# Kernel optimization log

Measured on AMD Instinct MI355X. Metric: run time of the kernel, lower is better.

Reference implementation:

```python
import jax, jax.numpy as jnp
import numpy as np

V, A, L = 10000, 600, 6          # dx vocab, num ancestors, ancestors-per-leaf
O, E = 128, 128                  # ontoEmbDim, EHREmbDim
ATD, PTD, DPL = 128, 128, 500    # ontoattnDim, ptattnDim, dpLabelSize
B, T, N = 64, 32, 40             # batch, visits, codes-per-visit


def _l2norm(x):
    return x / jnp.maximum(jnp.linalg.norm(x, axis=-1, keepdims=True), 1e-12)


def setup_inputs() -> dict:
    key = jax.random.key(0)
    ks = jax.random.split(key, 16)
    g = lambda k, shape, fan: (jax.random.normal(k, shape) / np.sqrt(fan)).astype(jnp.float32)
    dxseqs = jax.random.randint(ks[0], (B, T, N), 0, V + 1)          # V = padding idx
    dx_onehot = jax.random.uniform(ks[1], (T, B, V), dtype=jnp.float32)
    leaves = jax.random.randint(ks[2], (V, L), 0, V)
    ancestors = jax.random.randint(ks[3], (V, L), V, V + A)
    ehr_table = g(ks[4], (V + 1, E), E).at[V].set(0.0)               # padding row zero
    return dict(
        dxseqs=dxseqs, dx_onehot=dx_onehot, leaves=leaves, ancestors=ancestors,
        onto_table=g(ks[5], (V + A, O), O),
        onto_Wa=g(ks[6], (2 * O, ATD), 2 * O), onto_ba=jnp.zeros((ATD,), jnp.float32),
        onto_Wc=g(ks[7], (ATD, 1), ATD), onto_bc=jnp.zeros((1,), jnp.float32),
        ehr_table=ehr_table,
        attn_W=g(ks[8], (2 * E + 2 * O, PTD), 2 * E + 2 * O), attn_b=jnp.zeros((PTD,), jnp.float32),
        comb_W=g(ks[9], (PTD, 1), PTD), comb_b=jnp.zeros((1,), jnp.float32),
        co_W=g(ks[10], (E, V), E), co_b=jnp.zeros((V,), jnp.float32),
        dp_W=g(ks[11], (O + E, DPL), O + E), dp_b=jnp.zeros((DPL,), jnp.float32),
    )


def _forward(dxseqs, dx_onehot, leaves, ancestors, onto_table, onto_Wa, onto_ba,
             onto_Wc, onto_bc, ehr_table, attn_W, attn_b, comb_W, comb_b,
             co_W, co_b, dp_W, dp_b):
    # --- OntoEmb (GRAM-style ancestor attention) ---
    el = onto_table[leaves]                                  # (V, L, O)
    ea = onto_table[ancestors]                               # (V, L, O)
    h = jnp.tanh(jnp.concatenate([el, ea], -1) @ onto_Wa + onto_ba)
    a = jax.nn.softmax(h @ onto_Wc + onto_bc, axis=1)        # (V, L, 1)
    onto_all = jnp.concatenate(
        [jnp.sum(a * ea, axis=1), jnp.zeros((1, O), onto_table.dtype)], axis=0)  # (V+1, O)

    dxOnto = onto_all[dxseqs]                                # (B, T, N, O)
    ontoV = jnp.einsum('tbv,vo->bto', dx_onehot, onto_all[:-1])  # (B, T, O)
    dxEHR = ehr_table[dxseqs]                                # (B, T, N, E)
    ehrV = _l2norm(jnp.sum(dxEHR, axis=2))                   # (B, T, E)

    # --- cooccurrence branch ---
    cooccurU = jax.nn.softmax(ehrV @ co_W + co_b, axis=2)    # (B, T, V)
    vonehot = jnp.transpose(dx_onehot, (1, 0, 2))            # (B, T, V)
    cooccur_loss = -jnp.mean(jnp.sum(vonehot * jnp.log(cooccurU), axis=(1, 2)))

    # --- additive (Bahdanau) attention over codes in a visit ---
    dxEmb = jnp.concatenate([dxEHR, dxOnto], -1)             # (B, T, N, E+O)
    vs = jnp.concatenate([ontoV, ehrV], -1)[:, :, None, :]   # (B, T, 1, O+E)
    attnInput = jnp.concatenate([jnp.broadcast_to(vs, dxEmb.shape), dxEmb], -1)
    mlp = jnp.tanh(attnInput @ attn_W + attn_b)              # (B, T, N, PTD)
    attn = jax.nn.softmax(mlp @ comb_W + comb_b, axis=2)     # (B, T, N, 1)
    vs2 = jnp.sum(attn * dxEmb, axis=2)                      # (B, T, E+O)

    dp = jax.nn.softmax(jnp.tanh(_l2norm(vs2)) @ dp_W + dp_b, axis=2)  # (B, T, DPL)
    return dp, cooccur_loss * 10.0


def reference(dxseqs, dx_onehot, leaves, ancestors, onto_table, onto_Wa, onto_ba,
              onto_Wc, onto_bc, ehr_table, attn_W, attn_b, comb_W, comb_b,
              co_W, co_b, dp_W, dp_b):
    return _forward(dxseqs, dx_onehot, leaves, ancestors, onto_table, onto_Wa, onto_ba,
                    onto_Wc, onto_bc, ehr_table, attn_W, attn_b, comb_W, comb_b,
                    co_W, co_b, dp_W, dp_b)
```

## Files before the change

kernel.cpp:

```cpp
#include <hip/hip_runtime.h>
#include <math.h>

typedef float4 f4;
typedef __bf16 bf16x8 __attribute__((ext_vector_type(8)));
typedef float f32x4 __attribute__((ext_vector_type(4)));

static constexpr int kV = 10000, kL = 6, kDPL = 500;
static constexpr int kB = 64, kT = 32, kN = 40, kBT = 2048;
static constexpr int kXC = 5;
static constexpr int kNB = 272;
static constexpr int kLd = 10240;
static constexpr int kNP = 313;
static constexpr int kVT2 = 40;

#define MFMA16 __builtin_amdgcn_mfma_f32_16x16x32_bf16

typedef const __attribute__((address_space(1))) unsigned int ga_u32;
typedef __attribute__((address_space(3))) unsigned int lds_u32;
__device__ __forceinline__ void gll16(const float* g, float* l) {
  __builtin_amdgcn_global_load_lds((ga_u32*)g, (lds_u32*)l, 16, 0, 0);
}

__device__ __forceinline__ bf16x8 cvt8(f4 a, f4 b) {
  bf16x8 r;
  r[0] = (__bf16)a.x; r[1] = (__bf16)a.y; r[2] = (__bf16)a.z; r[3] = (__bf16)a.w;
  r[4] = (__bf16)b.x; r[5] = (__bf16)b.y; r[6] = (__bf16)b.z; r[7] = (__bf16)b.w;
  return r;
}

__global__ __launch_bounds__(256) void mmore_cvt_bf16(
    const float* __restrict__ in, __bf16* __restrict__ out, int n) {
  int i = (blockIdx.x * 256 + threadIdx.x) * 8;
  if (i < n) {
    f4 a = *(const f4*)(in + i), b = *(const f4*)(in + i + 4);
    *(bf16x8*)(out + i) = cvt8(a, b);
  }
}

__global__ __launch_bounds__(256) void mmore_trcvt(
    const float* __restrict__ in, __bf16* __restrict__ out,
    int K, int N, int Kpad) {
  int t = threadIdx.x;
  int n = blockIdx.y * 16 + (t & 15);
  int kb = (blockIdx.x * 16 + (t >> 4)) * 8;
  bf16x8 r;
  #pragma unroll
  for (int i = 0; i < 8; ++i) {
    int k = kb + i;
    float v = (k < K && n < N) ? in[(size_t)k * N + n] : 0.f;
    r[i] = (__bf16)v;
  }
  *(bf16x8*)(out + (size_t)n * Kpad + kb) = r;
}

__global__ __launch_bounds__(256) void mmore_brow(
    const float* __restrict__ coW, const float* __restrict__ cob,
    __bf16* __restrict__ Btab) {
  int id = blockIdx.x * 256 + threadIdx.x;
  int rr = id / 1280;
  int kk = (id - rr * 1280) * 8;
  bf16x8 r;
  #pragma unroll
  for (int i = 0; i < 8; ++i) {
    int k = kk + i;
    float v = 0.f;
    if (k < kV) {
      if (rr < 128) v = coW[(size_t)rr * kV + k];
      else if (rr == 128) v = cob[k];
      else if (rr == 129) v = 1.f;
    }
    r[i] = (__bf16)v;
  }
  *(bf16x8*)(Btab + (size_t)(128 + rr) * kLd + kk) = r;
}

__global__ __launch_bounds__(256) void mmore_panelize(
    const __bf16* __restrict__ Btab, __bf16* __restrict__ Bp) {
  int t = threadIdx.x;
  int S = blockIdx.x, ry = blockIdx.y;
  int row = ry * 16 + (t >> 4), kk = (t & 15) * 2;
  unsigned v = *(const unsigned*)(Btab + (size_t)row * kLd + S * 32 + kk);
  *(unsigned*)(Bp + ((size_t)S * kNB + row) * 32 + kk) = v;
}

__global__ __launch_bounds__(128) void mmore_ehrv(
    const int* __restrict__ dxseqs, const float* __restrict__ ehr_table,
    float* __restrict__ ehrV) {
  int bt = blockIdx.x, t = threadIdx.x;
  const int* row = dxseqs + bt * kN;
  float acc = 0.f;
  for (int n = 0; n < kN; ++n) acc += ehr_table[(size_t)row[n] * 128 + t];
  float v = acc * acc;
  #pragma unroll
  for (int off = 32; off; off >>= 1) v += __shfl_down(v, off);
  __shared__ float red[2];
  if ((t & 63) == 0) red[t >> 6] = v;
  __syncthreads();
  float ss = red[0] + red[1];
  float inv = 1.f / fmaxf(sqrtf(ss), 1e-12f);
  ehrV[bt * 128 + t] = acc * inv;
}

__global__ __launch_bounds__(256) void mmore_scores_mfma(
    const __bf16* __restrict__ otb, const int* __restrict__ leaves,
    const int* __restrict__ anc, const __bf16* __restrict__ WaT,
    const float* __restrict__ ba, const float* __restrict__ Wc,
    const float* __restrict__ bc, float* __restrict__ s_out) {
  int t = threadIdx.x, wave = t >> 6, lane = t & 63, lm = lane & 15, lg = lane >> 4;
  int r0 = blockIdx.x * 32;
  int rA0 = r0 + lm, rA1 = rA0 + 16;
  int v0 = rA0 / 6, l0 = rA0 - v0 * 6, v1 = rA1 / 6, l1 = rA1 - v1 * 6;
  const __bf16* pL0 = otb + (size_t)leaves[v0 * 6 + l0] * 128;
  const __bf16* pA0 = otb + (size_t)anc[v0 * 6 + l0] * 128;
  const __bf16* pL1 = otb + (size_t)leaves[v1 * 6 + l1] * 128;
  const __bf16* pA1 = otb + (size_t)anc[v1 * 6 + l1] * 128;
  const __bf16* bp = WaT + (size_t)(wave * 32 + lm) * 256 + lg * 8;
  f32x4 acc[2][2] = {};
  #pragma unroll
  for (int kb = 0; kb < 256; kb += 32) {
    int k = kb + lg * 8;
    const __bf16* s0 = (k < 128) ? (pL0 + k) : (pA0 + (k - 128));
    const __bf16* s1 = (k < 128) ? (pL1 + k) : (pA1 + (k - 128));
    bf16x8 a0 = *(const bf16x8*)s0;
    bf16x8 a1 = *(const bf16x8*)s1;
    bf16x8 b0 = *(const bf16x8*)(bp + kb);
    bf16x8 b1 = *(const bf16x8*)(bp + kb + 16 * 256);
    acc[0][0] = MFMA16(a0, b0, acc[0][0], 0, 0, 0);
    acc[0][1] = MFMA16(a0, b1, acc[0][1], 0, 0, 0);
    acc[1][0] = MFMA16(a1, b0, acc[1][0], 0, 0, 0);
    acc[1][1] = MFMA16(a1, b1, acc[1][1], 0, 0, 0);
  }
  __shared__ float red[4][32];
  float bcv = bc[0];
  #pragma unroll
  for (int mf = 0; mf < 2; ++mf) {
    #pragma unroll
    for (int j = 0; j < 4; ++j) {
      float p = 0.f;
      #pragma unroll
      for (int nf = 0; nf < 2; ++nf) {
        int c = wave * 32 + nf * 16 + lm;
        p += tanhf(acc[mf][nf][j] + ba[c]) * Wc[c];
      }
      #pragma unroll
      for (int off = 8; off; off >>= 1) p += __shfl_xor(p, off);
      if (lm == 0) red[wave][mf * 16 + lg * 4 + j] = p;
    }
  }
  __syncthreads();
  if (t < 32) s_out[r0 + t] = red[0][t] + red[1][t] + red[2][t] + red[3][t] + bcv;
}

__global__ __launch_bounds__(128) void mmore_onto(
    const float* __restrict__ ot, const int* __restrict__ anc,
    const float* __restrict__ s_in, float* __restrict__ onto_all) {
  int v = blockIdx.x, t = threadIdx.x;
  if (v == kV) { onto_all[(size_t)v * 128 + t] = 0.f; return; }
  __shared__ float sv[kL];
  __shared__ int aidx[kL];
  if (t < kL) { sv[t] = s_in[v * kL + t]; aidx[t] = anc[v * kL + t]; }
  __syncthreads();
  float mx = sv[0];
  #pragma unroll
  for (int l = 1; l < kL; ++l) mx = fmaxf(mx, sv[l]);
  float e[kL], sum = 0.f;
  #pragma unroll
  for (int l = 0; l < kL; ++l) { e[l] = expf(sv[l] - mx); sum += e[l]; }
  float acc = 0.f;
  #pragma unroll
  for (int l = 0; l < kL; ++l)
    acc += (e[l] / sum) * ot[(size_t)aidx[l] * 128 + t];
  onto_all[(size_t)v * 128 + t] = acc;
}

__global__ __launch_bounds__(256) void mmore_xgemm(
    const float* __restrict__ X, const __bf16* __restrict__ Bp,
    float* __restrict__ part) {
  __shared__ __align__(16) float Xs[2][16][256];
  int t = threadIdx.x, w = t >> 6, lane = t & 63, lm = lane & 15, lg = lane >> 4;
  int bid = blockIdx.x;
  int swz = (bid & 7) * 80 + (bid >> 3);
  int btile = swz & 127, chunk = swz >> 7;
  int r0 = btile * 16;
  bool lastc = (chunk == kXC - 1);
  int nSS = lastc ? 7 : 8;
  int kbase = chunk * 2048;
  int f0 = w * 4;
  const __bf16* bp = Bp + ((size_t)(chunk * 64) * kNB + lm) * 32 + lg * 8;
  f32x4 acc[5] = {};

#define XGV6_STAGE(db, S)                                                     \
  {                                                                           \
    _Pragma("unroll")                                                         \
    for (int u = 0; u < 4; ++u) {                                             \
      int row_ = w * 4 + u;                                                   \
      const float* src_ = X + (size_t)(r0 + row_) * kV + kbase + (S) * 256 +  \
                          ((lane ^ (row_ & 7)) << 2);                         \
      gll16(src_, &Xs[db][row_][0]);                                          \
    }                                                                         \
  }

  XGV6_STAGE(0, 0);
  asm volatile("s_waitcnt vmcnt(0)" ::: "memory");
  __builtin_amdgcn_s_barrier();
  int buf = 0;
  for (int S = 0; S < nSS; ++S) {
    if (S + 1 < nSS) {
      if (buf == 0) { XGV6_STAGE(1, S + 1); } else { XGV6_STAGE(0, S + 1); }
    }
    #pragma unroll
    for (int j = 0; j < 8; ++j) {
      int G0 = 8 * j + 2 * lg;
      int sw0 = G0 ^ (lm & 7), sw1 = (G0 + 1) ^ (lm & 7);
      f4 x0 = *(const f4*)&Xs[buf][lm][sw0 * 4];
      f4 x1 = *(const f4*)&Xs[buf][lm][sw1 * 4];
      bf16x8 af = cvt8(x0, x1);
      const __bf16* bs = bp + (size_t)(S * 8 + j) * (kNB * 32);
      acc[0] = MFMA16(af, *(const bf16x8*)(bs + (f0 + 0) * 512), acc[0], 0, 0, 0);
      acc[1] = MFMA16(af, *(const bf16x8*)(bs + (f0 + 1) * 512), acc[1], 0, 0, 0);
      acc[2] = MFMA16(af, *(const bf16x8*)(bs + (f0 + 2) * 512), acc[2], 0, 0, 0);
      acc[3] = MFMA16(af, *(const bf16x8*)(bs + (f0 + 3) * 512), acc[3], 0, 0, 0);
      if (w == 3)
        acc[4] = MFMA16(af, *(const bf16x8*)(bs + 16 * 512), acc[4], 0, 0, 0);
    }
    asm volatile("s_waitcnt vmcnt(0)" ::: "memory");
    __builtin_amdgcn_s_barrier();
    buf ^= 1;
  }
  if (lastc) {
    f4 z = make_float4(0.f, 0.f, 0.f, 0.f), x0 = z, x1 = z;
    if (lg < 2) {
      const float* xp = X + (size_t)(r0 + lm) * kV + 9984 + lg * 8;
      x0 = *(const f4*)xp; x1 = *(const f4*)(xp + 4);
    }
    bf16x8 af = cvt8(x0, x1);
    const __bf16* bs = Bp + ((size_t)312 * kNB + lm) * 32 + lg * 8;
    acc[0] = MFMA16(af, *(const bf16x8*)(bs + (f0 + 0) * 512), acc[0], 0, 0, 0);
    acc[1] = MFMA16(af, *(const bf16x8*)(bs + (f0 + 1) * 512), acc[1], 0, 0, 0);
    acc[2] = MFMA16(af, *(const bf16x8*)(bs + (f0 + 2) * 512), acc[2], 0, 0, 0);
    acc[3] = MFMA16(af, *(const bf16x8*)(bs + (f0 + 3) * 512), acc[3], 0, 0, 0);
    if (w == 3)
      acc[4] = MFMA16(af, *(const bf16x8*)(bs + 16 * 512), acc[4], 0, 0, 0);
  }
  #pragma unroll
  for (int j = 0; j < 4; ++j) {
    int r = r0 + lg * 4 + j;
    int bt = (r & 63) * kT + (r >> 6);
    size_t o = ((size_t)chunk * kBT + bt) * kNB;
    #pragma unroll
    for (int f = 0; f < 4; ++f) part[o + (f0 + f) * 16 + lm] = acc[f][j];
    if (w == 3) part[o + 256 + lm] = acc[4][j];
  }
#undef XGV6_STAGE
}

__global__ __launch_bounds__(256) void mmore_creduce(
    const float* __restrict__ part, float* __restrict__ ontoV,
    float* __restrict__ pwred, float* __restrict__ pc, float* __restrict__ sp) {
  int bt = blockIdx.x, t = threadIdx.x;
  for (int c = t; c < kNB; c += 256) {
    float a = 0.f;
    #pragma unroll
    for (int ch = 0; ch < kXC; ++ch)
      a += part[((size_t)ch * kBT + bt) * kNB + c];
    if (c < 128) ontoV[(size_t)bt * 128 + c] = a;
    else if (c < 256) pwred[(size_t)bt * 128 + (c - 128)] = a;
    else if (c == 256) pc[bt] = a;
    else if (c == 257) sp[bt] = a;
  }
}

__global__ __launch_bounds__(256) void mmore_lossg(
    const float* __restrict__ ehrV, const __bf16* __restrict__ coWT,
    const float* __restrict__ cob, float* __restrict__ epart) {
  int t = threadIdx.x, wave = t >> 6, lane = t & 63, lm = lane & 15, lg = lane >> 4;
  int vt = blockIdx.x, btile = blockIdx.y;
  int r0 = btile * 32, vb = vt * 256;
  const float* a0 = ehrV + (size_t)(r0 + lm) * 128 + lg * 8;
  const float* a1 = a0 + 16 * 128;
  f32x4 acc[2][4] = {};
  #pragma unroll
  for (int kb = 0; kb < 128; kb += 32) {
    f4 x0 = *(const f4*)(a0 + kb), x1 = *(const f4*)(a0 + kb + 4);
    f4 y0 = *(const f4*)(a1 + kb), y1 = *(const f4*)(a1 + kb + 4);
    bf16x8 af0 = cvt8(x0, x1), af1 = cvt8(y0, y1);
    #pragma unroll
    for (int nf = 0; nf < 4; ++nf) {
      int c = vb + wave * 64 + nf * 16 + lm;
      bf16x8 b = *(const bf16x8*)(coWT + (size_t)c * 128 + kb + lg * 8);
      acc[0][nf] = MFMA16(af0, b, acc[0][nf], 0, 0, 0);
      acc[1][nf] = MFMA16(af1, b, acc[1][nf], 0, 0, 0);
    }
  }
  float se[2][4] = {};
  #pragma unroll
  for (int nf = 0; nf < 4; ++nf) {
    int c = vb + wave * 64 + nf * 16 + lm;
    if (c < kV) {
      float cb = cob[c];
      #pragma unroll
      for (int mf = 0; mf < 2; ++mf)
        #pragma unroll
        for (int j = 0; j < 4; ++j)
          se[mf][j] += __expf(acc[mf][nf][j] + cb);
    }
  }
  __shared__ float red[4][32];
  #pragma unroll
  for (int mf = 0; mf < 2; ++mf)
    #pragma unroll
    for (int j = 0; j < 4; ++j) {
      float v = se[mf][j];
      #pragma unroll
      for (int off = 8; off; off >>= 1) v += __shfl_xor(v, off);
      if (lm == 0) red[wave][mf * 16 + lg * 4 + j] = v;
    }
  __syncthreads();
  if (t < 32)
    epart[(size_t)vt * kBT + r0 + t] =
        red[0][t] + red[1][t] + red[2][t] + red[3][t];
}

__global__ __launch_bounds__(256) void mmore_lossterm(
    const float* __restrict__ ehrV, const float* __restrict__ pwred,
    const float* __restrict__ pc, const float* __restrict__ sp,
    const float* __restrict__ epart, float* __restrict__ term) {
  int t = threadIdx.x;
  int bt = blockIdx.x * 16 + (t >> 4);
  int sub = t & 15;
  const f4* e = (const f4*)(ehrV + (size_t)bt * 128 + sub * 8);
  const f4* w = (const f4*)(pwred + (size_t)bt * 128 + sub * 8);
  f4 e0 = e[0], e1 = e[1], w0 = w[0], w1 = w[1];
  float d = e0.x * w0.x + e0.y * w0.y + e0.z * w0.z + e0.w * w0.w +
            e1.x * w1.x + e1.y * w1.y + e1.z * w1.z + e1.w * w1.w;
  float S = 0.f;
  for (int vt = sub; vt < kVT2; vt += 16) S += epart[(size_t)vt * kBT + bt];
  #pragma unroll
  for (int off = 8; off; off >>= 1) {
    d += __shfl_xor(d, off); S += __shfl_xor(S, off);
  }
  if (sub == 0) term[bt] = (d + pc[bt]) - sp[bt] * logf(S);
}

__global__ __launch_bounds__(256) void mmore_lossfin(
    const float* __restrict__ term, float* __restrict__ out) {
  int t = threadIdx.x;
  float a = 0.f;
  for (int i = t; i < kBT; i += 256) a += term[i];
  #pragma unroll
  for (int off = 32; off; off >>= 1) a += __shfl_down(a, off);
  __shared__ float red[4];
  if ((t & 63) == 0) red[t >> 6] = a;
  __syncthreads();
  if (t == 0) out[0] = -(10.f / 64.f) * (red[0] + red[1] + red[2] + red[3]);
}

__global__ __launch_bounds__(256) void mmore_gemm_mfma(
    const float* __restrict__ A, const __bf16* __restrict__ WT,
    int ldWT, int koff, const float* __restrict__ bias,
    float* __restrict__ C, int M, int accumulate) {
  int t = threadIdx.x, wave = t >> 6, lane = t & 63, lm = lane & 15, lg = lane >> 4;
  int r0 = blockIdx.x * 32;
  int row0 = r0 + lm, row1 = row0 + 16;
  bool ok0 = row0 < M, ok1 = row1 < M;
  const float* a0 = A + (size_t)row0 * 128 + lg * 8;
  const float* a1 = A + (size_t)row1 * 128 + lg * 8;
  const __bf16* bp = WT + (size_t)(wave * 32 + lm) * ldWT + koff + lg * 8;
  int ld16 = 16 * ldWT;
  f32x4 acc[2][2] = {};
  #pragma unroll
  for (int kb = 0; kb < 128; kb += 32) {
    f4 x0 = make_float4(0, 0, 0, 0), x1 = x0, y0 = x0, y1 = x0;
    if (ok0) { x0 = *(const f4*)(a0 + kb); x1 = *(const f4*)(a0 + kb + 4); }
    if (ok1) { y0 = *(const f4*)(a1 + kb); y1 = *(const f4*)(a1 + kb + 4); }
    bf16x8 af0 = cvt8(x0, x1), af1 = cvt8(y0, y1);
    bf16x8 b0 = *(const bf16x8*)(bp + kb);
    bf16x8 b1 = *(const bf16x8*)(bp + kb + ld16);
    acc[0][0] = MFMA16(af0, b0, acc[0][0], 0, 0, 0);
    acc[0][1] = MFMA16(af0, b1, acc[0][1], 0, 0, 0);
    acc[1][0] = MFMA16(af1, b0, acc[1][0], 0, 0, 0);
    acc[1][1] = MFMA16(af1, b1, acc[1][1], 0, 0, 0);
  }
  #pragma unroll
  for (int mf = 0; mf < 2; ++mf)
    #pragma unroll
    for (int nf = 0; nf < 2; ++nf) {
      int col = wave * 32 + nf * 16 + lm;
      #pragma unroll
      for (int j = 0; j < 4; ++j) {
        int row = r0 + mf * 16 + lg * 4 + j;
        if (row < M) {
          float v = acc[mf][nf][j];
          if (bias) v += bias[col];
          if (accumulate) v += C[(size_t)row * 128 + col];
          C[(size_t)row * 128 + col] = v;
        }
      }
    }
}

__device__ __forceinline__ float mmore_block_sum(float v, float* red) {
  int t = threadIdx.x;
  #pragma unroll
  for (int off = 32; off; off >>= 1) v += __shfl_down(v, off);
  if ((t & 63) == 0) red[t >> 6] = v;
  __syncthreads();
  if (t == 0) red[0] = red[0] + red[1] + red[2] + red[3];
  __syncthreads();
  return red[0];
}

__global__ __launch_bounds__(256) void mmore_attn(
    const int* __restrict__ dxseqs, const float* __restrict__ base,
    const float* __restrict__ pe, const float* __restrict__ po,
    const float* __restrict__ combW, const float* __restrict__ combB,
    const float* __restrict__ ehr_table, const float* __restrict__ onto_all,
    float* __restrict__ tn) {
  __shared__ float base_s[128];
  __shared__ int idx_s[kN];
  __shared__ float scp[kN][2];
  __shared__ float attn_s[64];
  __shared__ float red[4];
  int bt = blockIdx.x, t = threadIdx.x;
  if (t < 128) base_s[t] = base[bt * 128 + t];
  if (t < kN) idx_s[t] = dxseqs[bt * kN + t];
  __syncthreads();
  int c = t & 127, half = t >> 7, wid = t >> 6, lane = t & 63;
  float cw = combW[c];
  for (int n2 = 0; n2 < kN / 2; ++n2) {
    int n = n2 * 2 + half;
    int id = idx_s[n];
    float x = base_s[c] + pe[(size_t)id * 128 + c] + po[(size_t)id * 128 + c];
    float val = tanhf(x) * cw;
    #pragma unroll
    for (int off = 32; off; off >>= 1) val += __shfl_down(val, off);
    if (lane == 0) scp[n][wid & 1] = val;
  }
  __syncthreads();
  if (t < 64) {
    float s = (t < kN) ? (scp[t][0] + scp[t][1] + combB[0]) : -1e30f;
    float mx = s;
    #pragma unroll
    for (int off = 32; off; off >>= 1) mx = fmaxf(mx, __shfl_xor(mx, off));
    float e = (t < kN) ? __expf(s - mx) : 0.f;
    float sm = e;
    #pragma unroll
    for (int off = 32; off; off >>= 1) sm += __shfl_xor(sm, off);
    attn_s[t] = e / sm;
  }
  __syncthreads();
  float acc = 0.f;
  {
    const float* tab = (t < 128) ? ehr_table : onto_all;
    int j = t & 127;
    for (int n = 0; n < kN; ++n)
      acc += attn_s[n] * tab[(size_t)idx_s[n] * 128 + j];
  }
  float ss = mmore_block_sum(acc * acc, red);
  float inv = 1.f / fmaxf(sqrtf(ss), 1e-12f);
  tn[(size_t)bt * 256 + t] = tanhf(acc * inv);
}

__global__ __launch_bounds__(256) void mmore_dpgemm(
    const float* __restrict__ tn, const __bf16* __restrict__ dpWT,
    const float* __restrict__ dpB, float* __restrict__ u) {
  int t = threadIdx.x, wave = t >> 6, lane = t & 63, lm = lane & 15, lg = lane >> 4;
  int c0 = blockIdx.x * 128, r0 = blockIdx.y * 32;
  const float* a0 = tn + (size_t)(r0 + lm) * 256 + lg * 8;
  const float* a1 = a0 + 16 * 256;
  const __bf16* bp = dpWT + (size_t)(c0 + wave * 32 + lm) * 256 + lg * 8;
  f32x4 acc[2][2] = {};
  #pragma unroll
  for (int kb = 0; kb < 256; kb += 32) {
    f4 x0 = *(const f4*)(a0 + kb), x1 = *(const f4*)(a0 + kb + 4);
    f4 y0 = *(const f4*)(a1 + kb), y1 = *(const f4*)(a1 + kb + 4);
    bf16x8 af0 = cvt8(x0, x1), af1 = cvt8(y0, y1);
    bf16x8 b0 = *(const bf16x8*)(bp + kb);
    bf16x8 b1 = *(const bf16x8*)(bp + kb + 16 * 256);
    acc[0][0] = MFMA16(af0, b0, acc[0][0], 0, 0, 0);
    acc[0][1] = MFMA16(af0, b1, acc[0][1], 0, 0, 0);
    acc[1][0] = MFMA16(af1, b0, acc[1][0], 0, 0, 0);
    acc[1][1] = MFMA16(af1, b1, acc[1][1], 0, 0, 0);
  }
  #pragma unroll
  for (int mf = 0; mf < 2; ++mf)
    #pragma unroll
    for (int nf = 0; nf < 2; ++nf) {
      int col = c0 + wave * 32 + nf * 16 + lm;
      float bias = (col < kDPL) ? dpB[col] : 0.f;
      #pragma unroll
      for (int j = 0; j < 4; ++j) {
        int row = r0 + mf * 16 + lg * 4 + j;
        u[(size_t)row * 512 + col] = acc[mf][nf][j] + bias;
      }
    }
}

__global__ __launch_bounds__(128) void mmore_dpsoft(
    const float* __restrict__ u, float* __restrict__ out) {
  int bt = blockIdx.x, t = threadIdx.x;
  __shared__ float red[2];
  float v[4]; float mx = -1e30f;
  #pragma unroll
  for (int i = 0; i < 4; ++i) {
    int c = t + i * 128;
    v[i] = (c < kDPL) ? u[(size_t)bt * 512 + c] : -1e30f;
    mx = fmaxf(mx, v[i]);
  }
  #pragma unroll
  for (int off = 32; off; off >>= 1) mx = fmaxf(mx, __shfl_xor(mx, off));
  if ((t & 63) == 0) red[t >> 6] = mx;
  __syncthreads();
  mx = fmaxf(red[0], red[1]);
  __syncthreads();
  float e[4], s = 0.f;
  #pragma unroll
  for (int i = 0; i < 4; ++i) {
    int c = t + i * 128;
    e[i] = (c < kDPL) ? __expf(v[i] - mx) : 0.f;
    s += e[i];
  }
  #pragma unroll
  for (int off = 32; off; off >>= 1) s += __shfl_xor(s, off);
  if ((t & 63) == 0) red[t >> 6] = s;
  __syncthreads();
  float invS = 1.f / (red[0] + red[1]);
  #pragma unroll
  for (int i = 0; i < 4; ++i) {
    int c = t + i * 128;
    if (c < kDPL) out[(size_t)bt * kDPL + c] = e[i] * invS;
  }
}

extern "C" void kernel_launch(void* const* d_in, const int* in_sizes, int n_in,
                              void* d_out, int out_size, void* d_ws, size_t ws_size,
                              hipStream_t stream) {
  const int*   dxseqs     = (const int*)d_in[0];
  const float* dx_onehot  = (const float*)d_in[1];
  const int*   leaves     = (const int*)d_in[2];
  const int*   ancestors  = (const int*)d_in[3];
  const float* onto_table = (const float*)d_in[4];
  const float* onto_Wa    = (const float*)d_in[5];
  const float* onto_ba    = (const float*)d_in[6];
  const float* onto_Wc    = (const float*)d_in[7];
  const float* onto_bc    = (const float*)d_in[8];
  const float* ehr_table  = (const float*)d_in[9];
  const float* attn_W     = (const float*)d_in[10];
  const float* attn_b     = (const float*)d_in[11];
  const float* comb_W     = (const float*)d_in[12];
  const float* comb_b     = (const float*)d_in[13];
  const float* co_W       = (const float*)d_in[14];
  const float* co_b       = (const float*)d_in[15];
  const float* dp_W       = (const float*)d_in[16];
  const float* dp_b       = (const float*)d_in[17];
  float* out = (float*)d_out;

  float* ws = (float*)d_ws;
  size_t off = 0;
  auto alloc = [&](size_t n) { float* p = ws + off; off += n; return p; };
  float* onto_all = alloc((size_t)(kV + 1) * 128);
  float* s_sc     = alloc((size_t)kV * kL);
  float* ehrV     = alloc((size_t)kBT * 128);
  float* ontoV    = alloc((size_t)kBT * 128);
  __bf16* Bp      = (__bf16*)alloc((size_t)kNP * kNB * 32 / 2);
  __bf16* attn_WT = (__bf16*)alloc((size_t)128 * 512 / 2);
  __bf16* dpWT    = (__bf16*)alloc((size_t)512 * 256 / 2);
  __bf16* WaT     = (__bf16*)alloc((size_t)128 * 256 / 2);
  float* peR      = alloc((size_t)(kV + 1) * 128);
  float* poR      = alloc((size_t)(kV + 1) * 128);
  float* basep    = alloc((size_t)kBT * 128);
  float* epart    = alloc((size_t)kVT2 * kBT);
  float* pwred    = alloc((size_t)kBT * 128);
  float* pc       = alloc(kBT);
  float* sp       = alloc(kBT);
  float* term     = alloc(kBT);
  __bf16* ot_bf = (__bf16*)peR;
  __bf16* BtabL = (__bf16*)peR;
  float*  cpart = peR;
  __bf16* coWT  = (__bf16*)peR;
  float*  u     = peR;
  float*  tn    = ehrV;

  mmore_cvt_bf16<<<663, 256, 0, stream>>>(onto_table, ot_bf, 10600 * 128);
  mmore_trcvt<<<dim3(2, 8), 256, 0, stream>>>(onto_Wa, WaT, 256, 128, 256);
  mmore_trcvt<<<dim3(4, 8), 256, 0, stream>>>(attn_W, attn_WT, 512, 128, 512);
  mmore_trcvt<<<dim3(2, 32), 256, 0, stream>>>(dp_W, dpWT, 256, kDPL, 256);

  mmore_ehrv<<<kBT, 128, 0, stream>>>(dxseqs, ehr_table, ehrV);
  mmore_scores_mfma<<<(kV * kL) / 32, 256, 0, stream>>>(
      ot_bf, leaves, ancestors, WaT, onto_ba, onto_Wc, onto_bc, s_sc);
  mmore_onto<<<kV + 1, 128, 0, stream>>>(onto_table, ancestors, s_sc, onto_all);
  mmore_trcvt<<<dim3(80, 8), 256, 0, stream>>>(onto_all, BtabL, kV, 128, kLd);
  mmore_brow<<<720, 256, 0, stream>>>(co_W, co_b, BtabL);
  mmore_panelize<<<dim3(kNP, 17), 256, 0, stream>>>(BtabL, Bp);
  mmore_xgemm<<<128 * kXC, 256, 0, stream>>>(dx_onehot, Bp, cpart);
  mmore_creduce<<<kBT, 256, 0, stream>>>(cpart, ontoV, pwred, pc, sp);
  mmore_trcvt<<<dim3(1, 640), 256, 0, stream>>>(co_W, coWT, 128, kV, 128);
  mmore_lossg<<<dim3(kVT2, 64), 256, 0, stream>>>(ehrV, coWT, co_b, epart);
  mmore_lossterm<<<kBT / 16, 256, 0, stream>>>(ehrV, pwred, pc, sp, epart, term);
  mmore_lossfin<<<1, 256, 0, stream>>>(term, out + (size_t)kBT * kDPL);
  mmore_gemm_mfma<<<313, 256, 0, stream>>>(ehr_table, attn_WT, 512, 256, nullptr, peR, kV + 1, 0);
  mmore_gemm_mfma<<<313, 256, 0, stream>>>(onto_all, attn_WT, 512, 384, nullptr, poR, kV + 1, 0);
  mmore_gemm_mfma<<<64, 256, 0, stream>>>(ontoV, attn_WT, 512, 0, nullptr, basep, kBT, 0);
  mmore_gemm_mfma<<<64, 256, 0, stream>>>(ehrV, attn_WT, 512, 128, attn_b, basep, kBT, 1);
  mmore_attn<<<kBT, 256, 0, stream>>>(dxseqs, basep, peR, poR, comb_W, comb_b,
                                      ehr_table, onto_all, tn);
  mmore_dpgemm<<<dim3(4, 64), 256, 0, stream>>>(tn, dpWT, dp_b, u);
  mmore_dpsoft<<<kBT, 128, 0, stream>>>(u, out);
}
```

Baseline: 287.5 us.

## Double row tile per block in xgemm and lossg with 512-thread blocks

The xgemm kernel now processes 32 rows of the dense onehot matrix per block with 8 waves, so each B-panel fragment is shared across two row groups and the grid halves. The loss GEMM likewise covers 64 rows per block with 8 waves, each wave taking 16 rows by 128 columns, which changes how coWT loads are reused across rows. This aims to cut redundant B-matrix traffic and launch count. In exchange it doubles LDS staging in xgemm, and the smaller grids may lower occupancy.

```diff
diff --git a/kernel.cpp b/kernel.cpp
--- a/kernel.cpp
+++ b/kernel.cpp
@@ -173,23 +173,25 @@
   onto_all[(size_t)v * 128 + t] = acc;
 }
 
-__global__ __launch_bounds__(256) void mmore_xgemm(
+__global__ __launch_bounds__(512) void mmore_xgemm(
     const float* __restrict__ X, const __bf16* __restrict__ Bp,
     float* __restrict__ part) {
-  __shared__ __align__(16) float Xs[2][16][256];
+  __shared__ __align__(16) float Xs[2][32][256];
   int t = threadIdx.x, w = t >> 6, lane = t & 63, lm = lane & 15, lg = lane >> 4;
   int bid = blockIdx.x;
-  int swz = (bid & 7) * 80 + (bid >> 3);
-  int btile = swz & 127, chunk = swz >> 7;
-  int r0 = btile * 16;
+  int swz = (bid & 7) * 40 + (bid >> 3);
+  int btile = swz & 63, chunk = swz >> 6;
+  int r0 = btile * 32;
   bool lastc = (chunk == kXC - 1);
   int nSS = lastc ? 7 : 8;
   int kbase = chunk * 2048;
-  int f0 = w * 4;
+  int mf = w >> 2, f0 = (w & 3) * 4;
+  bool has16 = ((w & 3) == 3);
   const __bf16* bp = Bp + ((size_t)(chunk * 64) * kNB + lm) * 32 + lg * 8;
+  int rA = mf * 16 + lm;
   f32x4 acc[5] = {};
 
-#define XGV6_STAGE(db, S)                                                     \
+#define XGV7_STAGE(db, S)                                                     \
   {                                                                           \
     _Pragma("unroll")                                                         \
     for (int u = 0; u < 4; ++u) {                                             \
@@ -200,27 +202,27 @@
     }                                                                         \
   }
 
-  XGV6_STAGE(0, 0);
+  XGV7_STAGE(0, 0);
   asm volatile("s_waitcnt vmcnt(0)" ::: "memory");
   __builtin_amdgcn_s_barrier();
   int buf = 0;
   for (int S = 0; S < nSS; ++S) {
     if (S + 1 < nSS) {
-      if (buf == 0) { XGV6_STAGE(1, S + 1); } else { XGV6_STAGE(0, S + 1); }
+      if (buf == 0) { XGV7_STAGE(1, S + 1); } else { XGV7_STAGE(0, S + 1); }
     }
     #pragma unroll
     for (int j = 0; j < 8; ++j) {
       int G0 = 8 * j + 2 * lg;
-      int sw0 = G0 ^ (lm & 7), sw1 = (G0 + 1) ^ (lm & 7);
-      f4 x0 = *(const f4*)&Xs[buf][lm][sw0 * 4];
-      f4 x1 = *(const f4*)&Xs[buf][lm][sw1 * 4];
+      int sw0 = G0 ^ (rA & 7), sw1 = (G0 + 1) ^ (rA & 7);
+      f4 x0 = *(const f4*)&Xs[buf][rA][sw0 * 4];
+      f4 x1 = *(const f4*)&Xs[buf][rA][sw1 * 4];
       bf16x8 af = cvt8(x0, x1);
       const __bf16* bs = bp + (size_t)(S * 8 + j) * (kNB * 32);
       acc[0] = MFMA16(af, *(const bf16x8*)(bs + (f0 + 0) * 512), acc[0], 0, 0, 0);
       acc[1] = MFMA16(af, *(const bf16x8*)(bs + (f0 + 1) * 512), acc[1], 0, 0, 0);
       acc[2] = MFMA16(af, *(const bf16x8*)(bs + (f0 + 2) * 512), acc[2], 0, 0, 0);
       acc[3] = MFMA16(af, *(const bf16x8*)(bs + (f0 + 3) * 512), acc[3], 0, 0, 0);
-      if (w == 3)
+      if (has16)
         acc[4] = MFMA16(af, *(const bf16x8*)(bs + 16 * 512), acc[4], 0, 0, 0);
     }
     asm volatile("s_waitcnt vmcnt(0)" ::: "memory");
@@ -230,7 +232,7 @@
   if (lastc) {
     f4 z = make_float4(0.f, 0.f, 0.f, 0.f), x0 = z, x1 = z;
     if (lg < 2) {
-      const float* xp = X + (size_t)(r0 + lm) * kV + 9984 + lg * 8;
+      const float* xp = X + (size_t)(r0 + rA) * kV + 9984 + lg * 8;
       x0 = *(const f4*)xp; x1 = *(const f4*)(xp + 4);
     }
     bf16x8 af = cvt8(x0, x1);
@@ -239,19 +241,19 @@
     acc[1] = MFMA16(af, *(const bf16x8*)(bs + (f0 + 1) * 512), acc[1], 0, 0, 0);
     acc[2] = MFMA16(af, *(const bf16x8*)(bs + (f0 + 2) * 512), acc[2], 0, 0, 0);
     acc[3] = MFMA16(af, *(const bf16x8*)(bs + (f0 + 3) * 512), acc[3], 0, 0, 0);
-    if (w == 3)
+    if (has16)
       acc[4] = MFMA16(af, *(const bf16x8*)(bs + 16 * 512), acc[4], 0, 0, 0);
   }
   #pragma unroll
   for (int j = 0; j < 4; ++j) {
-    int r = r0 + lg * 4 + j;
+    int r = r0 + mf * 16 + lg * 4 + j;
     int bt = (r & 63) * kT + (r >> 6);
     size_t o = ((size_t)chunk * kBT + bt) * kNB;
     #pragma unroll
     for (int f = 0; f < 4; ++f) part[o + (f0 + f) * 16 + lm] = acc[f][j];
-    if (w == 3) part[o + 256 + lm] = acc[4][j];
-  }
-#undef XGV6_STAGE
+    if (has16) part[o + 256 + lm] = acc[4][j];
+  }
+#undef XGV7_STAGE
 }
 
 __global__ __launch_bounds__(256) void mmore_creduce(
@@ -270,55 +272,50 @@
   }
 }
 
-__global__ __launch_bounds__(256) void mmore_lossg(
+__global__ __launch_bounds__(512) void mmore_lossg(
     const float* __restrict__ ehrV, const __bf16* __restrict__ coWT,
     const float* __restrict__ cob, float* __restrict__ epart) {
-  int t = threadIdx.x, wave = t >> 6, lane = t & 63, lm = lane & 15, lg = lane >> 4;
+  int t = threadIdx.x, w = t >> 6, lane = t & 63, lm = lane & 15, lg = lane >> 4;
   int vt = blockIdx.x, btile = blockIdx.y;
-  int r0 = btile * 32, vb = vt * 256;
-  const float* a0 = ehrV + (size_t)(r0 + lm) * 128 + lg * 8;
-  const float* a1 = a0 + 16 * 128;
-  f32x4 acc[2][4] = {};
+  int r0 = btile * 64, vb = vt * 256;
+  int mf = w >> 1, ng = w & 1;
+  const float* a0 = ehrV + (size_t)(r0 + mf * 16 + lm) * 128 + lg * 8;
+  f32x4 acc[8] = {};
   #pragma unroll
   for (int kb = 0; kb < 128; kb += 32) {
     f4 x0 = *(const f4*)(a0 + kb), x1 = *(const f4*)(a0 + kb + 4);
-    f4 y0 = *(const f4*)(a1 + kb), y1 = *(const f4*)(a1 + kb + 4);
-    bf16x8 af0 = cvt8(x0, x1), af1 = cvt8(y0, y1);
-    #pragma unroll
-    for (int nf = 0; nf < 4; ++nf) {
-      int c = vb + wave * 64 + nf * 16 + lm;
+    bf16x8 af = cvt8(x0, x1);
+    #pragma unroll
+    for (int nf = 0; nf < 8; ++nf) {
+      int c = vb + ng * 128 + nf * 16 + lm;
       bf16x8 b = *(const bf16x8*)(coWT + (size_t)c * 128 + kb + lg * 8);
-      acc[0][nf] = MFMA16(af0, b, acc[0][nf], 0, 0, 0);
-      acc[1][nf] = MFMA16(af1, b, acc[1][nf], 0, 0, 0);
-    }
-  }
-  float se[2][4] = {};
-  #pragma unroll
-  for (int nf = 0; nf < 4; ++nf) {
-    int c = vb + wave * 64 + nf * 16 + lm;
+      acc[nf] = MFMA16(af, b, acc[nf], 0, 0, 0);
+    }
+  }
+  float se[4] = {};
+  #pragma unroll
+  for (int nf = 0; nf < 8; ++nf) {
+    int c = vb + ng * 128 + nf * 16 + lm;
     if (c < kV) {
       float cb = cob[c];
       #pragma unroll
-      for (int mf = 0; mf < 2; ++mf)
-        #pragma unroll
-        for (int j = 0; j < 4; ++j)
-          se[mf][j] += __expf(acc[mf][nf][j] + cb);
-    }
-  }
-  __shared__ float red[4][32];
-  #pragma unroll
-  for (int mf = 0; mf < 2; ++mf)
-    #pragma unroll
-    for (int j = 0; j < 4; ++j) {
-      float v = se[mf][j];
-      #pragma unroll
-      for (int off = 8; off; off >>= 1) v += __shfl_xor(v, off);
-      if (lm == 0) red[wave][mf * 16 + lg * 4 + j] = v;
-    }
-  __syncthreads();
-  if (t < 32)
-    epart[(size_t)vt * kBT + r0 + t] =
-        red[0][t] + red[1][t] + red[2][t] + red[3][t];
+      for (int j = 0; j < 4; ++j) se[j] += __expf(acc[nf][j] + cb);
+    }
+  }
+  __shared__ float red[8][16];
+  #pragma unroll
+  for (int j = 0; j < 4; ++j) {
+    float v = se[j];
+    #pragma unroll
+    for (int off = 8; off; off >>= 1) v += __shfl_xor(v, off);
+    if (lm == 0) red[w][lg * 4 + j] = v;
+  }
+  __syncthreads();
+  if (t < 64) {
+    int mf2 = t >> 4, i = t & 15;
+    epart[(size_t)vt * kBT + r0 + mf2 * 16 + i] =
+        red[mf2 * 2][i] + red[mf2 * 2 + 1][i];
+  }
 }
 
 __global__ __launch_bounds__(256) void mmore_lossterm(
@@ -593,10 +590,10 @@
   mmore_trcvt<<<dim3(80, 8), 256, 0, stream>>>(onto_all, BtabL, kV, 128, kLd);
   mmore_brow<<<720, 256, 0, stream>>>(co_W, co_b, BtabL);
   mmore_panelize<<<dim3(kNP, 17), 256, 0, stream>>>(BtabL, Bp);
-  mmore_xgemm<<<128 * kXC, 256, 0, stream>>>(dx_onehot, Bp, cpart);
+  mmore_xgemm<<<64 * kXC, 512, 0, stream>>>(dx_onehot, Bp, cpart);
   mmore_creduce<<<kBT, 256, 0, stream>>>(cpart, ontoV, pwred, pc, sp);
   mmore_trcvt<<<dim3(1, 640), 256, 0, stream>>>(co_W, coWT, 128, kV, 128);
-  mmore_lossg<<<dim3(kVT2, 64), 256, 0, stream>>>(ehrV, coWT, co_b, epart);
+  mmore_lossg<<<dim3(kVT2, 32), 512, 0, stream>>>(ehrV, coWT, co_b, epart);
   mmore_lossterm<<<kBT / 16, 256, 0, stream>>>(ehrV, pwred, pc, sp, epart, term);
   mmore_lossfin<<<1, 256, 0, stream>>>(term, out + (size_t)kBT * kDPL);
   mmore_gemm_mfma<<<313, 256, 0, stream>>>(ehr_table, attn_WT, 512, 256, nullptr, peR, kV + 1, 0);
```

Result: slower. 313.5 us (+9.1%).
